# Optimization experiments

Hardware: AMD Instinct MI355X
Metric: run time of the kernel (lower is better)

The kernel has to match this reference:

```python
import jax, jax.numpy as jnp
import numpy as np


def _dct_last(x):
    """Unnormalized DCT-II along the last axis via the FFT reorder+twiddle trick:
    v[n] = x[2n], v[N-1-n] = x[2n+1];  y[k] = Re( exp(-i*pi*k/(2N)) * FFT(v)[k] )
    => y[k] = sum_n x[n] * cos(pi*(2n+1)*k/(2N))
    This mirrors DREAMPlace's expk (twiddle) formulation.
    """
    N = x.shape[-1]
    v = jnp.concatenate([x[..., ::2], x[..., 1::2][..., ::-1]], axis=-1)
    V = jnp.fft.fft(v)
    k = jnp.arange(N)
    expk = jnp.exp(-1j * jnp.pi * k.astype(x.dtype) / (2.0 * N))
    return jnp.real(V * expk).astype(x.dtype)


def _dct2(x):
    # DCT-II along last axis, then along second-to-last axis (separable 2D DCT).
    y = _dct_last(x)
    y = _dct_last(jnp.swapaxes(y, -1, -2))
    return jnp.swapaxes(y, -1, -2)


def setup_inputs() -> dict:
    key = jax.random.key(0)
    x = jax.random.normal(key, (8, 2048, 2048), dtype=jnp.float32)
    return {"x": x}


def reference(x):
    return _dct2(x)
```

## Files before the change

kernel.cpp:

```cpp
#include <hip/hip_runtime.h>
#include <hip/hip_bf16.h>
#include <hip/hip_fp16.h>


typedef _Float16 half8 __attribute__((ext_vector_type(8)));
typedef float f32x4 __attribute__((ext_vector_type(4)));
typedef unsigned int uint32;

constexpr int BK = 32;
constexpr int BM = 256, BN = 256;
constexpr int KK = 1024;
constexpr int NT = KK / BK;
constexpr int TILE_E = BM * BK;

__device__ __forceinline__ unsigned short f2h_bits(float f) {
  _Float16 h = (_Float16)f;
  return __builtin_bit_cast(unsigned short, h);
}
__device__ __forceinline__ float h2f(unsigned short u) {
  return (float)__builtin_bit_cast(_Float16, u);
}

__device__ __forceinline__ void gload_lds16(const unsigned short* g, unsigned short* l) {
  __builtin_amdgcn_global_load_lds((const __attribute__((address_space(1))) void*)g,
                                   (__attribute__((address_space(3))) void*)l,
                                   16, 0, 0);
}

#define CFENCE asm volatile("" ::: "memory")

__device__ __forceinline__ int swz_idx(int r, int cbyte) {
  int b = (r >> 1) * 128 + ((((r & 1) << 6) | cbyte) ^ (((r >> 1) & 7) << 4));
  return b >> 1;
}

__device__ __forceinline__ void stage_tile(const unsigned short* __restrict__ G,
                                           int rowbase, int k0, int ld,
                                           unsigned short* lds, int wave, int lane) {
#pragma unroll
  for (int c = 0; c < 2; ++c) {
    const int p = c * 64 + wave * 8 + (lane >> 3);
    const int v = (lane & 7) ^ ((lane >> 3) & 7);
    const int r = 2 * p + (v >> 2);
    const int kslot = v & 3;
    const unsigned short* src = G + (size_t)(rowbase + r) * ld + (k0 + kslot * 8);
    unsigned short* dst = lds + (c * 64 + wave * 8) * 64;
    gload_lds16(src, dst);
  }
}

__global__ __launch_bounds__(256) void cvt_fold1(const float* __restrict__ x,
                                                 unsigned short* __restrict__ Xf) {
  int tid = blockIdx.x * 256 + threadIdx.x;
  int m = tid >> 7;
  int n0 = (tid & 127) << 3;
  const float* row = x + (size_t)m * 2048;
  float4 a = *(const float4*)(row + n0);
  float4 b = *(const float4*)(row + n0 + 4);
  float4 c = *(const float4*)(row + 2040 - n0);
  float4 d = *(const float4*)(row + 2044 - n0);
  float f[8] = {a.x, a.y, a.z, a.w, b.x, b.y, b.z, b.w};
  float g[8] = {d.w, d.z, d.y, d.x, c.w, c.z, c.y, c.x};
  uint32 up[4], um[4];
#pragma unroll
  for (int e = 0; e < 4; ++e) {
    up[e] = f2h_bits(f[2 * e] + g[2 * e]) |
            ((uint32)f2h_bits(f[2 * e + 1] + g[2 * e + 1]) << 16);
    um[e] = f2h_bits(f[2 * e] - g[2 * e]) |
            ((uint32)f2h_bits(f[2 * e + 1] - g[2 * e + 1]) << 16);
  }
  unsigned short* o = Xf + (size_t)m * 2048 + n0;
  *(uint4*)o = make_uint4(up[0], up[1], up[2], up[3]);
  *(uint4*)(o + 1024) = make_uint4(um[0], um[1], um[2], um[3]);
}

__global__ __launch_bounds__(256) void gen_cos2(unsigned short* __restrict__ Ce,
                                                unsigned short* __restrict__ Co) {
  int idx = blockIdx.x * 256 + threadIdx.x;
  int k = idx >> 10, n = idx & 1023;
  int tn = 2 * n + 1;
  int pe = (tn * (2 * k)) & 8191;
  int po = (tn * (2 * k + 1)) & 8191;
  const float s = 7.6699039394282061e-4f;
  Ce[idx] = f2h_bits(cosf((float)pe * s));
  Co[idx] = f2h_bits(cosf((float)po * s));
}

__global__ __launch_bounds__(256) void fold2(const unsigned short* __restrict__ Tt,
                                             unsigned short* __restrict__ U2) {
  int tid = blockIdx.x * 256 + threadIdx.x;
  int row = tid >> 7;
  int j = (tid & 127) << 3;
  const unsigned short* p = Tt + (size_t)row * 2048;
  uint4 F = *(const uint4*)(p + j);
  uint4 Bv = *(const uint4*)(p + 2040 - j);
  uint32 fw[4] = {F.x, F.y, F.z, F.w};
  uint32 bw[4] = {Bv.x, Bv.y, Bv.z, Bv.w};
  float fe[8], ge[8];
#pragma unroll
  for (int e = 0; e < 8; ++e) {
    fe[e] = h2f((unsigned short)(fw[e >> 1] >> ((e & 1) * 16)));
    int pi = 7 - e;
    ge[e] = h2f((unsigned short)(bw[pi >> 1] >> ((pi & 1) * 16)));
  }
  uint32 up[4], um[4];
#pragma unroll
  for (int e = 0; e < 4; ++e) {
    up[e] = f2h_bits(fe[2 * e] + ge[2 * e]) |
            ((uint32)f2h_bits(fe[2 * e + 1] + ge[2 * e + 1]) << 16);
    um[e] = f2h_bits(fe[2 * e] - ge[2 * e]) |
            ((uint32)f2h_bits(fe[2 * e + 1] - ge[2 * e + 1]) << 16);
  }
  unsigned short* o = U2 + (size_t)row * 2048 + j;
  *(uint4*)o = make_uint4(up[0], up[1], up[2], up[3]);
  *(uint4*)(o + 1024) = make_uint4(um[0], um[1], um[2], um[3]);
}

template <int MODE>
__global__ __launch_bounds__(512) void dct_gemm(
    const unsigned short* __restrict__ Ce, const unsigned short* __restrict__ Co,
    const unsigned short* __restrict__ D, void* __restrict__ outp) {
  __shared__ unsigned short As[4 * TILE_E];
  __shared__ unsigned short Bs[4 * TILE_E];

  const int tid = threadIdx.x;
  const int lane = tid & 63;
  const int wave = tid >> 6;
  const int wr = wave >> 2;
  const int wc = wave & 3;
  const int bm = blockIdx.y * BM;
  const int bn = blockIdx.x * BN;
  const int z = blockIdx.z;

  const unsigned short* Ag;
  const unsigned short* Bg;
  int lda, ldb, arow, brow;
  bool half;
  if (MODE == 0) {
    half = (bn >= 1024);
    Ag = D + (half ? 1024 : 0); lda = 2048; arow = bm;
    Bg = half ? Co : Ce;        ldb = 1024; brow = bn - (half ? 1024 : 0);
  } else {
    half = (bm >= 1024);
    Ag = half ? Co : Ce;        lda = 1024; arow = bm - (half ? 1024 : 0);
    Bg = D + (size_t)z * 4194304u + (half ? 1024 : 0);
    ldb = 2048; brow = bn;
  }

  const int frc = lane & 15;
  const int cb = (lane >> 4) << 4;

  f32x4 acc[8][4] = {};

  stage_tile(Ag, arow, 0, lda, &As[0], wave, lane);
  stage_tile(Bg, brow, 0, ldb, &Bs[0], wave, lane);
  stage_tile(Ag, arow, BK, lda, &As[TILE_E], wave, lane);
  stage_tile(Bg, brow, BK, ldb, &Bs[TILE_E], wave, lane);
  asm volatile("s_waitcnt vmcnt(4)" ::: "memory");
  CFENCE; __builtin_amdgcn_s_barrier(); CFENCE;

  for (int t = 0; t < NT; ++t) {
    const unsigned short* at = &As[(t & 3) * TILE_E];
    const unsigned short* bt = &Bs[(t & 3) * TILE_E];
    half8 af[4], bf[4];

#pragma unroll
    for (int m = 0; m < 4; ++m)
      af[m] = *(const half8*)&at[swz_idx(wr * 128 + m * 16 + frc, cb)];
#pragma unroll
    for (int n = 0; n < 4; ++n)
      bf[n] = *(const half8*)&bt[swz_idx(wc * 64 + n * 16 + frc, cb)];
    if (t + 2 < NT)
      stage_tile(Ag, arow, (t + 2) * BK, lda, &As[((t + 2) & 3) * TILE_E], wave, lane);
    CFENCE; __builtin_amdgcn_s_barrier(); CFENCE;
    __builtin_amdgcn_s_setprio(1);
#pragma unroll
    for (int m = 0; m < 4; ++m)
#pragma unroll
      for (int n = 0; n < 4; ++n)
        acc[m][n] = __builtin_amdgcn_mfma_f32_16x16x32_f16(af[m], bf[n], acc[m][n], 0, 0, 0);
    __builtin_amdgcn_s_setprio(0);

#pragma unroll
    for (int m = 0; m < 4; ++m)
      af[m] = *(const half8*)&at[swz_idx(wr * 128 + 64 + m * 16 + frc, cb)];
    if (t + 2 < NT)
      stage_tile(Bg, brow, (t + 2) * BK, ldb, &Bs[((t + 2) & 3) * TILE_E], wave, lane);
    if (t < NT - 2)
      asm volatile("s_waitcnt vmcnt(4)" ::: "memory");
    else if (t == NT - 2)
      asm volatile("s_waitcnt vmcnt(0)" ::: "memory");
    CFENCE; __builtin_amdgcn_s_barrier(); CFENCE;
    __builtin_amdgcn_s_setprio(1);
#pragma unroll
    for (int m = 0; m < 4; ++m)
#pragma unroll
      for (int n = 0; n < 4; ++n)
        acc[m + 4][n] =
            __builtin_amdgcn_mfma_f32_16x16x32_f16(af[m], bf[n], acc[m + 4][n], 0, 0, 0);
    __builtin_amdgcn_s_setprio(0);
  }

  const int koff = half ? 1024 : 0;
  if (MODE == 0) {
    unsigned short* Tt = (unsigned short*)outp;
#pragma unroll
    for (int mi = 0; mi < 8; ++mi) {
      const int r = bm + wr * 128 + (mi >> 2) * 64 + (mi & 3) * 16 + (lane >> 4) * 4;
      const int b = r >> 11;
      const int rb = r & 2047;
#pragma unroll
      for (int n = 0; n < 4; ++n) {
        const int cpk = bn + wc * 64 + n * 16 + frc;
        const int ktrue = 2 * (cpk - koff) + (half ? 1 : 0);
        uint32 lo = f2h_bits(acc[mi][n][0]) | ((uint32)f2h_bits(acc[mi][n][1]) << 16);
        uint32 hi = f2h_bits(acc[mi][n][2]) | ((uint32)f2h_bits(acc[mi][n][3]) << 16);
        *(uint2*)&Tt[(size_t)b * 4194304 + (size_t)ktrue * 2048 + rb] =
            make_uint2(lo, hi);
      }
    }
  } else {
    float* out = (float*)outp + (size_t)z * 4194304;
#pragma unroll
    for (int mi = 0; mi < 8; ++mi) {
      const int p0 =
          bm + wr * 128 + (mi >> 2) * 64 + (mi & 3) * 16 + (lane >> 4) * 4 - koff;
#pragma unroll
      for (int n = 0; n < 4; ++n) {
        const int cg = bn + wc * 64 + n * 16 + frc;
#pragma unroll
        for (int i = 0; i < 4; ++i) {
          const int rtrue = 2 * (p0 + i) + (half ? 1 : 0);
          out[(size_t)rtrue * 2048 + cg] = acc[mi][n][i];
        }
      }
    }
  }
}

extern "C" void kernel_launch(void* const* d_in, const int* in_sizes, int n_in,
                              void* d_out, int out_size, void* d_ws,
                              size_t ws_size, hipStream_t stream) {
  const float* x = (const float*)d_in[0];
  float* out = (float*)d_out;

  unsigned short* Xf = (unsigned short*)d_ws;
  unsigned short* Ce = Xf + 33554432u;
  unsigned short* Co = Ce + 1048576u;
  unsigned short* Tt = Co + 1048576u;

  cvt_fold1<<<8192, 256, 0, stream>>>(x, Xf);
  gen_cos2<<<4096, 256, 0, stream>>>(Ce, Co);
  dct_gemm<0><<<dim3(8, 64, 1), 512, 0, stream>>>(Ce, Co, Xf, (void*)Tt);
  fold2<<<8192, 256, 0, stream>>>(Tt, Xf);
  dct_gemm<1><<<dim3(8, 8, 8), 512, 0, stream>>>(Ce, Co, Xf, (void*)out);
}
```

Before: 229.7 us.

## Restructure GEMM main loop into 8-phase ping-pong schedule with split tile staging

Replaces the 4-stage BK=32 ring buffer with a double-buffered BK=64 scheme. Each 64-wide K step is split into eight MFMA phases of 4x2 fragments, and the global-to-LDS loads are spread as half-tiles between barriers. The aim is to interleave loads, LDS reads and MFMA clusters more finely, in the style of an hipBLASLt ping-pong schedule. In exchange it adds many more workgroup barriers per K step, and the reworked vmcnt waits could stall or break ordering.

```diff
diff --git a/kernel.cpp b/kernel.cpp
--- a/kernel.cpp
+++ b/kernel.cpp
@@ -7,11 +7,9 @@
 typedef float f32x4 __attribute__((ext_vector_type(4)));
 typedef unsigned int uint32;
 
-constexpr int BK = 32;
-constexpr int BM = 256, BN = 256;
 constexpr int KK = 1024;
-constexpr int NT = KK / BK;
-constexpr int TILE_E = BM * BK;
+constexpr int NITER = KK / 64;
+constexpr int SUB_E = 8192;
 
 __device__ __forceinline__ unsigned short f2h_bits(float f) {
   _Float16 h = (_Float16)f;
@@ -28,25 +26,23 @@
 }
 
 #define CFENCE asm volatile("" ::: "memory")
+#define BARRIER do { CFENCE; __builtin_amdgcn_s_barrier(); CFENCE; } while (0)
 
 __device__ __forceinline__ int swz_idx(int r, int cbyte) {
   int b = (r >> 1) * 128 + ((((r & 1) << 6) | cbyte) ^ (((r >> 1) & 7) << 4));
   return b >> 1;
 }
 
-__device__ __forceinline__ void stage_tile(const unsigned short* __restrict__ G,
+__device__ __forceinline__ void stage_half(const unsigned short* __restrict__ G,
                                            int rowbase, int k0, int ld,
-                                           unsigned short* lds, int wave, int lane) {
-#pragma unroll
-  for (int c = 0; c < 2; ++c) {
-    const int p = c * 64 + wave * 8 + (lane >> 3);
-    const int v = (lane & 7) ^ ((lane >> 3) & 7);
-    const int r = 2 * p + (v >> 2);
-    const int kslot = v & 3;
-    const unsigned short* src = G + (size_t)(rowbase + r) * ld + (k0 + kslot * 8);
-    unsigned short* dst = lds + (c * 64 + wave * 8) * 64;
-    gload_lds16(src, dst);
-  }
+                                           unsigned short* lds, int wave, int lane,
+                                           int c) {
+  const int p = c * 64 + wave * 8 + (lane >> 3);
+  const int v = (lane & 7) ^ ((lane >> 3) & 7);
+  const int r = 2 * p + (v >> 2);
+  const int kslot = v & 3;
+  gload_lds16(G + (size_t)(rowbase + r) * ld + (k0 + kslot * 8),
+              lds + (c * 64 + wave * 8) * 64);
 }
 
 __global__ __launch_bounds__(256) void cvt_fold1(const float* __restrict__ x,
@@ -120,16 +116,16 @@
 __global__ __launch_bounds__(512) void dct_gemm(
     const unsigned short* __restrict__ Ce, const unsigned short* __restrict__ Co,
     const unsigned short* __restrict__ D, void* __restrict__ outp) {
-  __shared__ unsigned short As[4 * TILE_E];
-  __shared__ unsigned short Bs[4 * TILE_E];
+  __shared__ unsigned short As[4 * SUB_E];
+  __shared__ unsigned short Bs[4 * SUB_E];
 
   const int tid = threadIdx.x;
   const int lane = tid & 63;
   const int wave = tid >> 6;
   const int wr = wave >> 2;
   const int wc = wave & 3;
-  const int bm = blockIdx.y * BM;
-  const int bn = blockIdx.x * BN;
+  const int bm = blockIdx.y * 256;
+  const int bn = blockIdx.x * 256;
   const int z = blockIdx.z;
 
   const unsigned short* Ag;
@@ -152,53 +148,144 @@
 
   f32x4 acc[8][4] = {};
 
-  stage_tile(Ag, arow, 0, lda, &As[0], wave, lane);
-  stage_tile(Bg, brow, 0, ldb, &Bs[0], wave, lane);
-  stage_tile(Ag, arow, BK, lda, &As[TILE_E], wave, lane);
-  stage_tile(Bg, brow, BK, ldb, &Bs[TILE_E], wave, lane);
+  stage_half(Ag, arow, 0, lda, &As[0 * SUB_E], wave, lane, 0);
+  stage_half(Ag, arow, 0, lda, &As[0 * SUB_E], wave, lane, 1);
+  stage_half(Bg, brow, 0, ldb, &Bs[0 * SUB_E], wave, lane, 0);
+  stage_half(Bg, brow, 0, ldb, &Bs[0 * SUB_E], wave, lane, 1);
+  stage_half(Ag, arow, 32, lda, &As[1 * SUB_E], wave, lane, 0);
+  stage_half(Ag, arow, 32, lda, &As[1 * SUB_E], wave, lane, 1);
+  stage_half(Bg, brow, 32, ldb, &Bs[1 * SUB_E], wave, lane, 0);
+  stage_half(Bg, brow, 32, ldb, &Bs[1 * SUB_E], wave, lane, 1);
   asm volatile("s_waitcnt vmcnt(4)" ::: "memory");
-  CFENCE; __builtin_amdgcn_s_barrier(); CFENCE;
-
-  for (int t = 0; t < NT; ++t) {
-    const unsigned short* at = &As[(t & 3) * TILE_E];
-    const unsigned short* bt = &Bs[(t & 3) * TILE_E];
-    half8 af[4], bf[4];
-
-#pragma unroll
-    for (int m = 0; m < 4; ++m)
-      af[m] = *(const half8*)&at[swz_idx(wr * 128 + m * 16 + frc, cb)];
-#pragma unroll
-    for (int n = 0; n < 4; ++n)
-      bf[n] = *(const half8*)&bt[swz_idx(wc * 64 + n * 16 + frc, cb)];
-    if (t + 2 < NT)
-      stage_tile(Ag, arow, (t + 2) * BK, lda, &As[((t + 2) & 3) * TILE_E], wave, lane);
-    CFENCE; __builtin_amdgcn_s_barrier(); CFENCE;
-    __builtin_amdgcn_s_setprio(1);
-#pragma unroll
-    for (int m = 0; m < 4; ++m)
-#pragma unroll
-      for (int n = 0; n < 4; ++n)
-        acc[m][n] = __builtin_amdgcn_mfma_f32_16x16x32_f16(af[m], bf[n], acc[m][n], 0, 0, 0);
-    __builtin_amdgcn_s_setprio(0);
-
-#pragma unroll
-    for (int m = 0; m < 4; ++m)
-      af[m] = *(const half8*)&at[swz_idx(wr * 128 + 64 + m * 16 + frc, cb)];
-    if (t + 2 < NT)
-      stage_tile(Bg, brow, (t + 2) * BK, ldb, &Bs[((t + 2) & 3) * TILE_E], wave, lane);
-    if (t < NT - 2)
+  BARRIER;
+
+  for (int i = 0; i < NITER; ++i) {
+    const int b = i & 1;
+    const unsigned short* a0 = &As[(b * 2 + 0) * SUB_E];
+    const unsigned short* a1 = &As[(b * 2 + 1) * SUB_E];
+    const unsigned short* bt0 = &Bs[(b * 2 + 0) * SUB_E];
+    const unsigned short* bt1 = &Bs[(b * 2 + 1) * SUB_E];
+    unsigned short* nA0 = &As[((b ^ 1) * 2 + 0) * SUB_E];
+    unsigned short* nA1 = &As[((b ^ 1) * 2 + 1) * SUB_E];
+    unsigned short* nB0 = &Bs[((b ^ 1) * 2 + 0) * SUB_E];
+    unsigned short* nB1 = &Bs[((b ^ 1) * 2 + 1) * SUB_E];
+    const int kn = (i + 1) * 64;
+    const bool st = (i + 1 < NITER);
+
+    half8 af[4], bf0[2], bf1[2];
+
+#pragma unroll
+    for (int m = 0; m < 4; ++m)
+      af[m] = *(const half8*)&a0[swz_idx(wr * 128 + m * 16 + frc, cb)];
+#pragma unroll
+    for (int n = 0; n < 2; ++n)
+      bf0[n] = *(const half8*)&bt0[swz_idx(wc * 64 + n * 16 + frc, cb)];
+    if (st) stage_half(Ag, arow, kn, lda, nA0, wave, lane, 0);
+    BARRIER;
+    __builtin_amdgcn_s_setprio(1);
+#pragma unroll
+    for (int m = 0; m < 4; ++m)
+#pragma unroll
+      for (int n = 0; n < 2; ++n)
+        acc[m][n] = __builtin_amdgcn_mfma_f32_16x16x32_f16(af[m], bf0[n], acc[m][n], 0, 0, 0);
+    __builtin_amdgcn_s_setprio(0);
+    BARRIER;
+#pragma unroll
+    for (int n = 0; n < 2; ++n)
+      bf1[n] = *(const half8*)&bt0[swz_idx(wc * 64 + (n + 2) * 16 + frc, cb)];
+    if (st) stage_half(Ag, arow, kn, lda, nA0, wave, lane, 1);
+    BARRIER;
+    __builtin_amdgcn_s_setprio(1);
+#pragma unroll
+    for (int m = 0; m < 4; ++m)
+#pragma unroll
+      for (int n = 0; n < 2; ++n)
+        acc[m][n + 2] = __builtin_amdgcn_mfma_f32_16x16x32_f16(af[m], bf1[n], acc[m][n + 2], 0, 0, 0);
+    __builtin_amdgcn_s_setprio(0);
+    BARRIER;
+#pragma unroll
+    for (int m = 0; m < 4; ++m)
+      af[m] = *(const half8*)&a0[swz_idx(wr * 128 + 64 + m * 16 + frc, cb)];
+    if (st) stage_half(Bg, brow, kn, ldb, nB0, wave, lane, 0);
+    BARRIER;
+    __builtin_amdgcn_s_setprio(1);
+#pragma unroll
+    for (int m = 0; m < 4; ++m)
+#pragma unroll
+      for (int n = 0; n < 2; ++n)
+        acc[m + 4][n] = __builtin_amdgcn_mfma_f32_16x16x32_f16(af[m], bf0[n], acc[m + 4][n], 0, 0, 0);
+    __builtin_amdgcn_s_setprio(0);
+    BARRIER;
+    if (st) stage_half(Bg, brow, kn, ldb, nB0, wave, lane, 1);
+    if (st)
       asm volatile("s_waitcnt vmcnt(4)" ::: "memory");
-    else if (t == NT - 2)
+    else
       asm volatile("s_waitcnt vmcnt(0)" ::: "memory");
-    CFENCE; __builtin_amdgcn_s_barrier(); CFENCE;
-    __builtin_amdgcn_s_setprio(1);
-#pragma unroll
-    for (int m = 0; m < 4; ++m)
-#pragma unroll
-      for (int n = 0; n < 4; ++n)
-        acc[m + 4][n] =
-            __builtin_amdgcn_mfma_f32_16x16x32_f16(af[m], bf[n], acc[m + 4][n], 0, 0, 0);
-    __builtin_amdgcn_s_setprio(0);
+    BARRIER;
+    __builtin_amdgcn_s_setprio(1);
+#pragma unroll
+    for (int m = 0; m < 4; ++m)
+#pragma unroll
+      for (int n = 0; n < 2; ++n)
+        acc[m + 4][n + 2] = __builtin_amdgcn_mfma_f32_16x16x32_f16(af[m], bf1[n], acc[m + 4][n + 2], 0, 0, 0);
+    __builtin_amdgcn_s_setprio(0);
+    BARRIER;
+
+#pragma unroll
+    for (int m = 0; m < 4; ++m)
+      af[m] = *(const half8*)&a1[swz_idx(wr * 128 + m * 16 + frc, cb)];
+#pragma unroll
+    for (int n = 0; n < 2; ++n)
+      bf0[n] = *(const half8*)&bt1[swz_idx(wc * 64 + n * 16 + frc, cb)];
+    if (st) stage_half(Ag, arow, kn + 32, lda, nA1, wave, lane, 0);
+    BARRIER;
+    __builtin_amdgcn_s_setprio(1);
+#pragma unroll
+    for (int m = 0; m < 4; ++m)
+#pragma unroll
+      for (int n = 0; n < 2; ++n)
+        acc[m][n] = __builtin_amdgcn_mfma_f32_16x16x32_f16(af[m], bf0[n], acc[m][n], 0, 0, 0);
+    __builtin_amdgcn_s_setprio(0);
+    BARRIER;
+#pragma unroll
+    for (int n = 0; n < 2; ++n)
+      bf1[n] = *(const half8*)&bt1[swz_idx(wc * 64 + (n + 2) * 16 + frc, cb)];
+    if (st) stage_half(Ag, arow, kn + 32, lda, nA1, wave, lane, 1);
+    BARRIER;
+    __builtin_amdgcn_s_setprio(1);
+#pragma unroll
+    for (int m = 0; m < 4; ++m)
+#pragma unroll
+      for (int n = 0; n < 2; ++n)
+        acc[m][n + 2] = __builtin_amdgcn_mfma_f32_16x16x32_f16(af[m], bf1[n], acc[m][n + 2], 0, 0, 0);
+    __builtin_amdgcn_s_setprio(0);
+    BARRIER;
+#pragma unroll
+    for (int m = 0; m < 4; ++m)
+      af[m] = *(const half8*)&a1[swz_idx(wr * 128 + 64 + m * 16 + frc, cb)];
+    if (st) stage_half(Bg, brow, kn + 32, ldb, nB1, wave, lane, 0);
+    BARRIER;
+    __builtin_amdgcn_s_setprio(1);
+#pragma unroll
+    for (int m = 0; m < 4; ++m)
+#pragma unroll
+      for (int n = 0; n < 2; ++n)
+        acc[m + 4][n] = __builtin_amdgcn_mfma_f32_16x16x32_f16(af[m], bf0[n], acc[m + 4][n], 0, 0, 0);
+    __builtin_amdgcn_s_setprio(0);
+    BARRIER;
+    if (st) {
+      stage_half(Bg, brow, kn + 32, ldb, nB1, wave, lane, 1);
+      asm volatile("s_waitcnt vmcnt(4)" ::: "memory");
+    }
+    BARRIER;
+    __builtin_amdgcn_s_setprio(1);
+#pragma unroll
+    for (int m = 0; m < 4; ++m)
+#pragma unroll
+      for (int n = 0; n < 2; ++n)
+        acc[m + 4][n + 2] = __builtin_amdgcn_mfma_f32_16x16x32_f16(af[m], bf1[n], acc[m + 4][n + 2], 0, 0, 0);
+    __builtin_amdgcn_s_setprio(0);
+    BARRIER;
   }
 
   const int koff = half ? 1024 : 0;
```

New measurement: 237.6 us. 1.03x slower.

## Fold both DCT axes up front and drop the intermediate fold2 pass

Applied to the files above, without the earlier changes.

The even/odd fold along the second axis now happens in the input conversion kernel, which reads mirrored row pairs and writes the four sum/difference combinations at once. Because the fold commutes with the first-axis GEMM, the separate fold2 kernel, with its extra read and write of the fp16 intermediate, is removed. The second GEMM reads the first GEMM's output directly. The trade-offs are more memory traffic per thread in the first kernel, and correctness depends on the output layout of the first GEMM matching what the second GEMM now expects.

```diff
diff --git a/kernel.cpp b/kernel.cpp
--- a/kernel.cpp
+++ b/kernel.cpp
@@ -16,9 +16,6 @@
 __device__ __forceinline__ unsigned short f2h_bits(float f) {
   _Float16 h = (_Float16)f;
   return __builtin_bit_cast(unsigned short, h);
-}
-__device__ __forceinline__ float h2f(unsigned short u) {
-  return (float)__builtin_bit_cast(_Float16, u);
 }
 
 __device__ __forceinline__ void gload_lds16(const unsigned short* g, unsigned short* l) {
@@ -49,29 +46,47 @@
   }
 }
 
-__global__ __launch_bounds__(256) void cvt_fold1(const float* __restrict__ x,
-                                                 unsigned short* __restrict__ Xf) {
+__global__ __launch_bounds__(256) void cvt_fold12(const float* __restrict__ x,
+                                                  unsigned short* __restrict__ Xff) {
   int tid = blockIdx.x * 256 + threadIdx.x;
   int m = tid >> 7;
-  int n0 = (tid & 127) << 3;
-  const float* row = x + (size_t)m * 2048;
-  float4 a = *(const float4*)(row + n0);
-  float4 b = *(const float4*)(row + n0 + 4);
-  float4 c = *(const float4*)(row + 2040 - n0);
-  float4 d = *(const float4*)(row + 2044 - n0);
-  float f[8] = {a.x, a.y, a.z, a.w, b.x, b.y, b.z, b.w};
-  float g[8] = {d.w, d.z, d.y, d.x, c.w, c.z, c.y, c.x};
-  uint32 up[4], um[4];
+  int b = m >> 10;
+  int ui = m & 1023;
+  int j0 = (tid & 127) << 3;
+  const float* rf = x + ((size_t)b * 2048 + ui) * 2048;
+  const float* rb = x + ((size_t)b * 2048 + 2047 - ui) * 2048;
+  float4 fa = *(const float4*)(rf + j0);
+  float4 fb = *(const float4*)(rf + j0 + 4);
+  float4 fc = *(const float4*)(rf + 2040 - j0);
+  float4 fd = *(const float4*)(rf + 2044 - j0);
+  float4 ga = *(const float4*)(rb + j0);
+  float4 gb = *(const float4*)(rb + j0 + 4);
+  float4 gc = *(const float4*)(rb + 2040 - j0);
+  float4 gd = *(const float4*)(rb + 2044 - j0);
+  float f[8] = {fa.x, fa.y, fa.z, fa.w, fb.x, fb.y, fb.z, fb.w};
+  float fm[8] = {fd.w, fd.z, fd.y, fd.x, fc.w, fc.z, fc.y, fc.x};
+  float g[8] = {ga.x, ga.y, ga.z, ga.w, gb.x, gb.y, gb.z, gb.w};
+  float gm[8] = {gd.w, gd.z, gd.y, gd.x, gc.w, gc.z, gc.y, gc.x};
+  uint32 ss[4], sd[4], ds[4], dd[4];
 #pragma unroll
   for (int e = 0; e < 4; ++e) {
-    up[e] = f2h_bits(f[2 * e] + g[2 * e]) |
-            ((uint32)f2h_bits(f[2 * e + 1] + g[2 * e + 1]) << 16);
-    um[e] = f2h_bits(f[2 * e] - g[2 * e]) |
-            ((uint32)f2h_bits(f[2 * e + 1] - g[2 * e + 1]) << 16);
-  }
-  unsigned short* o = Xf + (size_t)m * 2048 + n0;
-  *(uint4*)o = make_uint4(up[0], up[1], up[2], up[3]);
-  *(uint4*)(o + 1024) = make_uint4(um[0], um[1], um[2], um[3]);
+#pragma unroll
+    for (int h = 0; h < 2; ++h) {
+      int k = 2 * e + h;
+      float fs = f[k] + fm[k], fdv = f[k] - fm[k];
+      float gs = g[k] + gm[k], gdv = g[k] - gm[k];
+      uint32 vss = f2h_bits(fs + gs), vsd = f2h_bits(fdv + gdv);
+      uint32 vds = f2h_bits(fs - gs), vdd = f2h_bits(fdv - gdv);
+      if (h == 0) { ss[e] = vss; sd[e] = vsd; ds[e] = vds; dd[e] = vdd; }
+      else { ss[e] |= vss << 16; sd[e] |= vsd << 16; ds[e] |= vds << 16; dd[e] |= vdd << 16; }
+    }
+  }
+  unsigned short* os = Xff + ((size_t)b * 2048 + ui) * 2048 + j0;
+  unsigned short* od = Xff + ((size_t)b * 2048 + 1024 + ui) * 2048 + j0;
+  *(uint4*)os = make_uint4(ss[0], ss[1], ss[2], ss[3]);
+  *(uint4*)(os + 1024) = make_uint4(sd[0], sd[1], sd[2], sd[3]);
+  *(uint4*)od = make_uint4(ds[0], ds[1], ds[2], ds[3]);
+  *(uint4*)(od + 1024) = make_uint4(dd[0], dd[1], dd[2], dd[3]);
 }
 
 __global__ __launch_bounds__(256) void gen_cos2(unsigned short* __restrict__ Ce,
@@ -84,36 +99,6 @@
   const float s = 7.6699039394282061e-4f;
   Ce[idx] = f2h_bits(cosf((float)pe * s));
   Co[idx] = f2h_bits(cosf((float)po * s));
-}
-
-__global__ __launch_bounds__(256) void fold2(const unsigned short* __restrict__ Tt,
-                                             unsigned short* __restrict__ U2) {
-  int tid = blockIdx.x * 256 + threadIdx.x;
-  int row = tid >> 7;
-  int j = (tid & 127) << 3;
-  const unsigned short* p = Tt + (size_t)row * 2048;
-  uint4 F = *(const uint4*)(p + j);
-  uint4 Bv = *(const uint4*)(p + 2040 - j);
-  uint32 fw[4] = {F.x, F.y, F.z, F.w};
-  uint32 bw[4] = {Bv.x, Bv.y, Bv.z, Bv.w};
-  float fe[8], ge[8];
-#pragma unroll
-  for (int e = 0; e < 8; ++e) {
-    fe[e] = h2f((unsigned short)(fw[e >> 1] >> ((e & 1) * 16)));
-    int pi = 7 - e;
-    ge[e] = h2f((unsigned short)(bw[pi >> 1] >> ((pi & 1) * 16)));
-  }
-  uint32 up[4], um[4];
-#pragma unroll
-  for (int e = 0; e < 4; ++e) {
-    up[e] = f2h_bits(fe[2 * e] + ge[2 * e]) |
-            ((uint32)f2h_bits(fe[2 * e + 1] + ge[2 * e + 1]) << 16);
-    um[e] = f2h_bits(fe[2 * e] - ge[2 * e]) |
-            ((uint32)f2h_bits(fe[2 * e + 1] - ge[2 * e + 1]) << 16);
-  }
-  unsigned short* o = U2 + (size_t)row * 2048 + j;
-  *(uint4*)o = make_uint4(up[0], up[1], up[2], up[3]);
-  *(uint4*)(o + 1024) = make_uint4(um[0], um[1], um[2], um[3]);
 }
 
 template <int MODE>
@@ -203,7 +188,7 @@
 
   const int koff = half ? 1024 : 0;
   if (MODE == 0) {
-    unsigned short* Tt = (unsigned short*)outp;
+    unsigned short* U2t = (unsigned short*)outp;
 #pragma unroll
     for (int mi = 0; mi < 8; ++mi) {
       const int r = bm + wr * 128 + (mi >> 2) * 64 + (mi & 3) * 16 + (lane >> 4) * 4;
@@ -215,7 +200,7 @@
         const int ktrue = 2 * (cpk - koff) + (half ? 1 : 0);
         uint32 lo = f2h_bits(acc[mi][n][0]) | ((uint32)f2h_bits(acc[mi][n][1]) << 16);
         uint32 hi = f2h_bits(acc[mi][n][2]) | ((uint32)f2h_bits(acc[mi][n][3]) << 16);
-        *(uint2*)&Tt[(size_t)b * 4194304 + (size_t)ktrue * 2048 + rb] =
+        *(uint2*)&U2t[(size_t)b * 4194304 + (size_t)ktrue * 2048 + rb] =
             make_uint2(lo, hi);
       }
     }
@@ -244,14 +229,13 @@
   const float* x = (const float*)d_in[0];
   float* out = (float*)d_out;
 
-  unsigned short* Xf = (unsigned short*)d_ws;
-  unsigned short* Ce = Xf + 33554432u;
+  unsigned short* Xff = (unsigned short*)d_ws;
+  unsigned short* Ce = Xff + 33554432u;
   unsigned short* Co = Ce + 1048576u;
-  unsigned short* Tt = Co + 1048576u;
-
-  cvt_fold1<<<8192, 256, 0, stream>>>(x, Xf);
+  unsigned short* U2t = Co + 1048576u;
+
+  cvt_fold12<<<4096, 256, 0, stream>>>(x, Xff);
   gen_cos2<<<4096, 256, 0, stream>>>(Ce, Co);
-  dct_gemm<0><<<dim3(8, 64, 1), 512, 0, stream>>>(Ce, Co, Xf, (void*)Tt);
-  fold2<<<8192, 256, 0, stream>>>(Tt, Xf);
-  dct_gemm<1><<<dim3(8, 8, 8), 512, 0, stream>>>(Ce, Co, Xf, (void*)out);
-}
+  dct_gemm<0><<<dim3(8, 64, 1), 512, 0, stream>>>(Ce, Co, Xff, (void*)U2t);
+  dct_gemm<1><<<dim3(8, 8, 8), 512, 0, stream>>>(Ce, Co, U2t, (void*)out);
+}
```

Result: faster. 208.5 us (-9.2%).
